# Kernel tuning notes

Measured on AMD Instinct MI355X. Metric: run time of the kernel, lower is better.

## Reference

```python
import jax, jax.numpy as jnp
import numpy as np

B, H1, W1 = 2, 64, 64
H2, W2 = 64, 64
DIM = 64    # query_latent_dim
CLD = 128   # cost_latent_dim
K = 8       # latent tokens in cost memory
HEADS = 8
CH = 1      # cost_heads_num
R = 4


def layer_norm(x, g, b, eps=1e-5):
    m = x.mean(-1, keepdims=True)
    v = ((x - m) ** 2).mean(-1, keepdims=True)
    return (x - m) / jnp.sqrt(v + eps) * g + b


def lin_pos_emb(x, dim):
    # LinearPositionEmbeddingSine: x [N,1,2] -> [N,1,dim]
    freq = jnp.linspace(0.0, dim // 4 - 1, dim // 4)
    a = 3.14 * x[..., 0:1] * freq / 200.0
    b = 3.14 * x[..., 1:2] * freq / 200.0
    return jnp.concatenate([jnp.sin(a), jnp.cos(a), jnp.sin(b), jnp.cos(b)], axis=-1)


def bilinear_sample(img, coords):
    # img: [N,C,H,W]; coords: [N,h,w,2] (x,y) pixel coords; zero padding, align_corners=True
    N, C, H, W = img.shape
    x, y = coords[..., 0], coords[..., 1]
    x0 = jnp.floor(x); y0 = jnp.floor(y)
    wx = x - x0; wy = y - y0
    nidx = jnp.arange(N)[:, None, None]

    def gather(xi, yi):
        valid = ((xi >= 0) & (xi <= W - 1) & (yi >= 0) & (yi <= H - 1)).astype(img.dtype)
        xc = jnp.clip(xi, 0, W - 1).astype(jnp.int32)
        yc = jnp.clip(yi, 0, H - 1).astype(jnp.int32)
        return img[nidx, :, yc, xc] * valid[..., None]  # [N,h,w,C]

    v00 = gather(x0, y0); v10 = gather(x0 + 1.0, y0)
    v01 = gather(x0, y0 + 1.0); v11 = gather(x0 + 1.0, y0 + 1.0)
    out = (v00 * ((1 - wx) * (1 - wy))[..., None] + v10 * (wx * (1 - wy))[..., None]
           + v01 * ((1 - wx) * wy)[..., None] + v11 * (wx * wy)[..., None])
    return out.transpose(0, 3, 1, 2)  # [N,C,h,w]


def encode_flow(cost_maps, coords1):
    b, _, h1, w1 = coords1.shape
    c = coords1.transpose(0, 2, 3, 1)  # [B,H1,W1,2]
    d = jnp.linspace(-float(R), float(R), 2 * R + 1)
    dy, dx = jnp.meshgrid(d, d, indexing='ij')
    delta = jnp.stack([dy, dx], axis=-1)  # [9,9,2]
    centroid = c.reshape(b * h1 * w1, 1, 1, 2)
    samp = centroid + delta[None]  # [B*H1*W1,9,9,2]
    corr = bilinear_sample(cost_maps, samp)  # [B*H1*W1,CH,9,9]
    return corr.reshape(b, h1, w1, -1).transpose(0, 3, 1, 2)  # [B,81*CH,H1,W1]


def upsample_flow(flow, mask):
    # convex upsample [H,W] -> [8H,8W]
    n, _, h, w = flow.shape
    m = jax.nn.softmax(mask.reshape(n, 1, 9, 8, 8, h, w), axis=2)
    f = jnp.pad(8.0 * flow, ((0, 0), (0, 0), (1, 1), (1, 1)))
    patches = jnp.stack([f[:, :, i:i + h, j:j + w] for i in range(3) for j in range(3)], axis=2)
    up = jnp.sum(m * patches[:, :, :, None, None], axis=2)  # [N,2,8,8,H,W]
    return up.transpose(0, 1, 4, 2, 5, 3).reshape(n, 2, 8 * h, 8 * w)


def setup_inputs() -> dict:
    key = jax.random.key(0)
    ks = jax.random.split(key, 16)
    Bn = B * H1 * W1
    ys, xs = np.meshgrid(np.arange(H1), np.arange(W1), indexing='ij')
    grid = jnp.asarray(np.stack([xs, ys], 0), jnp.float32)  # [2,H1,W1], (x,y)
    coords1 = jnp.broadcast_to(grid, (B, 2, H1, W1)) + 3.0 * jax.random.normal(ks[0], (B, 2, H1, W1), jnp.float32)
    s = 0.05
    return {
        'cost_maps': jax.random.normal(ks[1], (Bn, CH, H2, W2), jnp.float32),
        'cost_memory': jax.random.normal(ks[2], (Bn, K, CLD), jnp.float32),
        'coords1': coords1,
        'up_mask': jax.random.normal(ks[3], (B, 9 * 64, H1, W1), jnp.float32),
        'fte_w1': s * jax.random.normal(ks[4], (DIM, 81 * CH), jnp.float32),
        'fte_b1': jnp.zeros((DIM,), jnp.float32),
        'fte_w2': s * jax.random.normal(ks[5], (DIM, DIM), jnp.float32),
        'fte_b2': jnp.zeros((DIM,), jnp.float32),
        'ln1_g': jnp.ones((DIM,), jnp.float32),
        'ln1_b': jnp.zeros((DIM,), jnp.float32),
        'ln2_g': jnp.ones((DIM,), jnp.float32),
        'ln2_b': jnp.zeros((DIM,), jnp.float32),
        'wq': s * jax.random.normal(ks[6], (DIM, DIM), jnp.float32),
        'bq': jnp.zeros((DIM,), jnp.float32),
        'wk': s * jax.random.normal(ks[7], (CLD, DIM), jnp.float32),
        'bk': jnp.zeros((DIM,), jnp.float32),
        'wv': s * jax.random.normal(ks[8], (CLD, DIM), jnp.float32),
        'bv': jnp.zeros((DIM,), jnp.float32),
        'wp': s * jax.random.normal(ks[9], (2 * DIM, DIM), jnp.float32),
        'bp': jnp.zeros((DIM,), jnp.float32),
        'ffn_w1': s * jax.random.normal(ks[10], (DIM, DIM), jnp.float32),
        'ffn_b1': jnp.zeros((DIM,), jnp.float32),
        'ffn_w2': s * jax.random.normal(ks[11], (DIM, DIM), jnp.float32),
        'ffn_b2': jnp.zeros((DIM,), jnp.float32),
    }


def reference(cost_maps, cost_memory, coords1, up_mask,
              fte_w1, fte_b1, fte_w2, fte_b2,
              ln1_g, ln1_b, ln2_g, ln2_b,
              wq, bq, wk, bk, wv, bv, wp, bp,
              ffn_w1, ffn_b1, ffn_w2, ffn_b2):
    Bn = B * H1 * W1
    ys, xs = jnp.meshgrid(jnp.arange(H1, dtype=coords1.dtype), jnp.arange(W1, dtype=coords1.dtype), indexing='ij')
    coords0 = jnp.broadcast_to(jnp.stack([xs, ys], 0), (B, 2, H1, W1))

    # correlation-volume bilinear sampling (encode_flow_token)
    corr = encode_flow(cost_maps, coords1)  # [B,81*CH,H1,W1]

    # flow token encoder: 1x1 conv -> GELU -> 1x1 conv
    q = jnp.einsum('bchw,oc->bohw', corr, fte_w1) + fte_b1[None, :, None, None]
    q = jax.nn.gelu(q, approximate=False)
    q = jnp.einsum('bchw,oc->bohw', q, fte_w2) + fte_b2[None, :, None, None]
    query = q.transpose(0, 2, 3, 1).reshape(Bn, 1, DIM)

    # cross attention with linear sine position encoding of query coords
    qc = coords1.reshape(B, 2, H1 * W1).transpose(0, 2, 1).reshape(Bn, 1, 2)
    enc = lin_pos_emb(qc, DIM)
    short = query
    qn = layer_norm(query, ln1_g, ln1_b)
    qlin = (qn + enc) @ wq + bq            # [Bn,1,DIM]
    k = cost_memory @ wk + bk              # [Bn,K,DIM]
    v = cost_memory @ wv + bv
    hd = DIM // HEADS
    qh = qlin.reshape(Bn, 1, HEADS, hd).transpose(0, 2, 1, 3)
    kh = k.reshape(Bn, K, HEADS, hd).transpose(0, 2, 1, 3)
    vh = v.reshape(Bn, K, HEADS, hd).transpose(0, 2, 1, 3)
    attn = jax.nn.softmax(jnp.einsum('bhid,bhjd->bhij', qh, kh) * (hd ** -0.5), axis=-1)
    out = jnp.einsum('bhij,bhjd->bhid', attn, vh).transpose(0, 2, 1, 3).reshape(Bn, 1, DIM)
    x = jnp.concatenate([out, short], -1) @ wp + bp
    x = short + x
    xn = layer_norm(x, ln2_g, ln2_b)
    x = x + (jax.nn.gelu(xn @ ffn_w1 + ffn_b1, approximate=False) @ ffn_w2 + ffn_b2)
    cost_global = x.reshape(B, H1, W1, DIM).transpose(0, 3, 1, 2)

    # convex upsampling of the flow field
    flow_up = upsample_flow(coords1 - coords0, up_mask)  # [B,2,8*H1,8*W1]
    return (flow_up, cost_global)
```

## Files before the change

kernel.cpp:

```cpp
#include <hip/hip_runtime.h>
#include <math.h>

typedef _Float16 h2 __attribute__((ext_vector_type(2)));

#if __has_builtin(__builtin_amdgcn_fdot2)
#define FDOT2(a,b,c) __builtin_amdgcn_fdot2((a),(b),(c),false)
#else
__device__ __forceinline__ float FDOT2(h2 a, h2 b, float c){
    return c + (float)a.x*(float)b.x + (float)a.y*(float)b.y;
}
#endif

__device__ __forceinline__ h2 pk2(float x, float y){
#if __has_builtin(__builtin_amdgcn_cvt_pkrtz)
    return __builtin_bit_cast(h2, __builtin_amdgcn_cvt_pkrtz(x, y));
#else
    h2 r; r.x = (_Float16)x; r.y = (_Float16)y; return r;
#endif
}
__device__ __forceinline__ unsigned h2u(h2 v){ return __builtin_bit_cast(unsigned, v); }
__device__ __forceinline__ h2 uh2(unsigned v){ return __builtin_bit_cast(h2, v); }

__device__ __forceinline__ float fast_rcp(float x){
#if __has_builtin(__builtin_amdgcn_rcpf)
    return __builtin_amdgcn_rcpf(x);
#else
    return 1.f/x;
#endif
}

__device__ __forceinline__ float dot8(uint4 w, uint4 v, float acc){
    acc = FDOT2(uh2(w.x), uh2(v.x), acc);
    acc = FDOT2(uh2(w.y), uh2(v.y), acc);
    acc = FDOT2(uh2(w.z), uh2(v.z), acc);
    acc = FDOT2(uh2(w.w), uh2(v.w), acc);
    return acc;
}

__device__ __forceinline__ float gelu_exact(float x){
    return 0.5f * x * (1.0f + erff(x * 0.70710678118654752f));
}

__device__ __forceinline__ void ln_stats(float x, float& mean, float& inv){
    float s1 = x, s2 = x*x;
    #pragma unroll
    for(int off = 32; off >= 1; off >>= 1){
        s1 += __shfl_xor(s1, off, 64);
        s2 += __shfl_xor(s2, off, 64);
    }
    mean = s1 * (1.f/64.f);
    float var = fmaxf(s2 * (1.f/64.f) - mean*mean, 0.f);
    inv = rsqrtf(var + 1e-5f);
}

__device__ __forceinline__ void lds_fence(){ __asm__ volatile("s_waitcnt lgkmcnt(0)" ::: "memory"); }

#define W1T_OFF 0
#define W2T_OFF 2816
#define WQ_OFF  5120
#define FW1_OFF 7424
#define FW2_OFF 9728
#define WV_OFF  12032
#define WP_OFF  16384
#define WK_OFF  20736
#define WTOT    25344

#define CMO   0
#define TUO   544
#define CORRO 1088
#define QPO   1132
#define CCO   1168
#define PIXDW 1232
#define LDSDW (WTOT + 8*PIXDW)

__global__ void prep_weights(const float* __restrict__ w1, const float* __restrict__ w2,
                             const float* __restrict__ wq, const float* __restrict__ fw1,
                             const float* __restrict__ fw2, const float* __restrict__ wv,
                             const float* __restrict__ wp, const float* __restrict__ wk,
                             unsigned* __restrict__ ws){
    int idx = blockIdx.x * blockDim.x + threadIdx.x;
    if(idx >= WTOT) return;
    float a = 0.f, b = 0.f;
    if(idx < W2T_OFF){
        int t = idx / 44, cp = idx % 44;
        if(2*cp   < 81) a = w1[t*81 + 2*cp];
        if(2*cp+1 < 81) b = w1[t*81 + 2*cp+1];
    } else if(idx < WQ_OFF){
        int r = idx - W2T_OFF; int t = r / 36, cp = r % 36;
        if(cp < 32){ a = w2[t*64 + 2*cp]; b = w2[t*64 + 2*cp+1]; }
    } else if(idx < FW1_OFF){
        int r = idx - WQ_OFF; int t = r / 36, cp = r % 36;
        if(cp < 32){ a = wq[(2*cp)*64 + t]; b = wq[(2*cp+1)*64 + t]; }
    } else if(idx < FW2_OFF){
        int r = idx - FW1_OFF; int t = r / 36, cp = r % 36;
        if(cp < 32){ a = fw1[(2*cp)*64 + t]; b = fw1[(2*cp+1)*64 + t]; }
    } else if(idx < WV_OFF){
        int r = idx - FW2_OFF; int t = r / 36, cp = r % 36;
        if(cp < 32){ a = fw2[(2*cp)*64 + t]; b = fw2[(2*cp+1)*64 + t]; }
    } else if(idx < WP_OFF){
        int r = idx - WV_OFF; int t = r / 68, cp = r % 68;
        if(cp < 64){ a = wv[(2*cp)*64 + t]; b = wv[(2*cp+1)*64 + t]; }
    } else if(idx < WK_OFF){
        int r = idx - WP_OFF; int t = r / 68, cp = r % 68;
        if(cp < 64){ a = wp[(2*cp)*64 + t]; b = wp[(2*cp+1)*64 + t]; }
    } else {
        int r = idx - WK_OFF; int c = r / 36, hp = r % 36;
        if(hp < 32){ a = wk[c*64 + 2*hp]; b = wk[c*64 + 2*hp+1]; }
    }
    ws[idx] = h2u(pk2(a, b));
}

__device__ __forceinline__ float bilin(const float* __restrict__ cmap, float cx, float cy, int e){
    int i = e / 9, j = e - 9*i;
    float sx = cx + (float)(i - 4);
    float sy = cy + (float)(j - 4);
    float x0 = floorf(sx), y0 = floorf(sy);
    float wx = sx - x0,   wy = sy - y0;
    float acc = 0.f;
    #pragma unroll
    for(int dy = 0; dy < 2; dy++){
        #pragma unroll
        for(int dx = 0; dx < 2; dx++){
            float xf = x0 + (float)dx, yf = y0 + (float)dy;
            bool valid = (xf >= 0.f) && (xf <= 63.f) && (yf >= 0.f) && (yf <= 63.f);
            int xi = min(max((int)xf, 0), 63);
            int yi = min(max((int)yf, 0), 63);
            float v = valid ? cmap[yi*64 + xi] : 0.f;
            acc += v * ((dx ? wx : 1.f - wx) * (dy ? wy : 1.f - wy));
        }
    }
    return acc;
}

__global__ __launch_bounds__(512, 1) void decoder_main(
    const float* __restrict__ cost_maps, const float* __restrict__ cost_memory,
    const float* __restrict__ coords1, const unsigned* __restrict__ ws,
    const float* __restrict__ fte_b1, const float* __restrict__ fte_b2,
    const float* __restrict__ ln1_g, const float* __restrict__ ln1_b,
    const float* __restrict__ ln2_g, const float* __restrict__ ln2_b,
    const float* __restrict__ bq, const float* __restrict__ bv,
    const float* __restrict__ bp, const float* __restrict__ fb1,
    const float* __restrict__ fb2, float* __restrict__ out_cg)
{
    __shared__ unsigned sm[LDSDW];

    const int tid = threadIdx.x;
    const int wv  = tid >> 6;
    const int ln  = tid & 63;

    {
        const uint4* src = (const uint4*)ws;
        uint4* dst = (uint4*)sm;
        for(int i = tid; i < WTOT/4; i += 512) dst[i] = src[i];
    }
    const float b1v = fte_b1[ln], b2v = fte_b2[ln];
    const float g1v = ln1_g[ln], be1 = ln1_b[ln];
    const float g2v = ln2_g[ln], be2 = ln2_b[ln];
    const float bqv = bq[ln], bvv = bv[ln], bpv = bp[ln];
    const float f1v = fb1[ln], f2v = fb2[ln];
    __syncthreads();

    unsigned* P = sm + WTOT + wv * PIXDW;

    const int h_ = ln & 7;
    const int c0 = ln >> 3;
    const int j_ = ln >> 3;
    const int h3 = ln >> 3;

    int pix = blockIdx.x * 32 + wv;
    const float4* cm4p = (const float4*)cost_memory;
    float4 cmv0 = cm4p[(size_t)pix*256 +   0 + ln];
    float4 cmv1 = cm4p[(size_t)pix*256 +  64 + ln];
    float4 cmv2 = cm4p[(size_t)pix*256 + 128 + ln];
    float4 cmv3 = cm4p[(size_t)pix*256 + 192 + ln];
    float cx = coords1[(pix >> 12)*8192 + (pix & 4095)];
    float cy = coords1[(pix >> 12)*8192 + 4096 + (pix & 4095)];

    #pragma unroll 1
    for(int g = 0; g < 4; g++){
        {
            float4 v; int l0, jt, cp0;
            #define STAGE(V, I4) \
                v = V; l0 = 4*((I4)*64 + ln); jt = l0 >> 7; cp0 = (l0 & 127) >> 1; \
                { uint2 pw; pw.x = h2u(pk2(v.x, v.y)); pw.y = h2u(pk2(v.z, v.w)); \
                  *(uint2*)&P[CMO + jt*68 + cp0] = pw; }
            STAGE(cmv0, 0) STAGE(cmv1, 1) STAGE(cmv2, 2) STAGE(cmv3, 3)
            #undef STAGE
        }
        {
            const float* cmap = cost_maps + (size_t)pix * 4096;
            float cv = bilin(cmap, cx, cy, ln);
            float c2 = bilin(cmap, cx, cy, 64 + ln);
            float pr = __shfl_xor(cv, 1, 64);
            if((ln & 1) == 0) P[CORRO + (ln >> 1)] = h2u(pk2(cv, pr));
            float pr2 = __shfl_xor(c2, 1, 64);
            if(ln < 17 && (ln & 1) == 0){
                float bb = (ln == 16) ? 0.f : pr2;
                P[CORRO + 32 + (ln >> 1)] = h2u(pk2(c2, bb));
            }
            if(ln < 3) P[CORRO + 41 + ln] = 0u;
        }
        int npix = pix + 8;
        float4 n0, n1, n2, n3; float ncx = 0.f, ncy = 0.f;
        if(g < 3){
            n0 = cm4p[(size_t)npix*256 +   0 + ln];
            n1 = cm4p[(size_t)npix*256 +  64 + ln];
            n2 = cm4p[(size_t)npix*256 + 128 + ln];
            n3 = cm4p[(size_t)npix*256 + 192 + ln];
            ncx = coords1[(npix >> 12)*8192 + (npix & 4095)];
            ncy = coords1[(npix >> 12)*8192 + 4096 + (npix & 4095)];
        }
        lds_fence();

        float q1;
        {
            const uint4* wr = (const uint4*)&sm[W1T_OFF + ln*44];
            const uint4* ar = (const uint4*)&P[CORRO];
            float a0 = b1v, a1 = 0.f;
            #pragma unroll
            for(int gg = 0; gg < 10; gg += 2){
                a0 = dot8(wr[gg],   ar[gg],   a0);
                a1 = dot8(wr[gg+1], ar[gg+1], a1);
            }
            a0 = dot8(wr[10], ar[10], a0);
            q1 = a0 + a1;
        }
        q1 = gelu_exact(q1);
        {
            float pr = __shfl_xor(q1, 1, 64);
            if((ln & 1) == 0) P[QPO + (ln >> 1)] = h2u(pk2(q1, pr));
        }
        lds_fence();
        float shortv;
        {
            const uint4* wr = (const uint4*)&sm[W2T_OFF + ln*36];
            const uint4* ar = (const uint4*)&P[QPO];
            float a0 = b2v, a1 = 0.f;
            #pragma unroll
            for(int gg = 0; gg < 8; gg += 2){
                a0 = dot8(wr[gg],   ar[gg],   a0);
                a1 = dot8(wr[gg+1], ar[gg+1], a1);
            }
            shortv = a0 + a1;
        }
        {
            float psv = __shfl_xor(shortv, 1, 64);
            if((ln & 1) == 0) P[CCO + 32 + (ln >> 1)] = h2u(pk2(shortv, psv));
        }
        float mean, inv1;
        ln_stats(shortv, mean, inv1);
        float qn = (shortv - mean) * inv1 * g1v + be1;
        {
            int   fi    = ln & 15;
            float coord = (ln < 32) ? cx : cy;
            float ang   = 3.14f * coord * (float)fi / 200.0f;
            float enc   = (ln & 16) ? __cosf(ang) : __sinf(ang);
            float qv    = qn + enc;
            float pr = __shfl_xor(qv, 1, 64);
            if((ln & 1) == 0) P[QPO + (ln >> 1)] = h2u(pk2(qv, pr));
        }
        lds_fence();
        float qlin;
        {
            const uint4* wr = (const uint4*)&sm[WQ_OFF + ln*36];
            const uint4* ar = (const uint4*)&P[QPO];
            float a0 = bqv, a1 = 0.f;
            #pragma unroll
            for(int gg = 0; gg < 8; gg += 2){
                a0 = dot8(wr[gg],   ar[gg],   a0);
                a1 = dot8(wr[gg+1], ar[gg+1], a1);
            }
            qlin = a0 + a1;
        }
        (void)qlin;
        {
            uint4 qh4 = *(const uint4*)&P[QPO + h_*4];
            #pragma unroll
            for(int i = 0; i < 16; i++){
                int c = c0 + 8*i;
                uint4 wk4 = *(const uint4*)&sm[WK_OFF + c*36 + h_*4];
                float tv = dot8(wk4, qh4, 0.f);
                float prt = __shfl_xor(tv, 8, 64);
                if((c0 & 1) == 0) P[TUO + h_*68 + (c0 >> 1) + 4*i] = h2u(pk2(tv, prt));
            }
        }
        lds_fence();
        float sacc;
        {
            const int hk = ln & 7;
            const uint4* cmr = (const uint4*)&P[CMO + j_*68];
            const uint4* tur = (const uint4*)&P[TUO + hk*68];
            float s0 = 0.f, s1 = 0.f, s2 = 0.f, s3 = 0.f;
            #pragma unroll
            for(int gg = 0; gg < 16; gg += 4){
                s0 = dot8(cmr[gg],   tur[gg],   s0);
                s1 = dot8(cmr[gg+1], tur[gg+1], s1);
                s2 = dot8(cmr[gg+2], tur[gg+2], s2);
                s3 = dot8(cmr[gg+3], tur[gg+3], s3);
            }
            sacc = (s0 + s1) + (s2 + s3);
        }
        float p;
        {
            float sc = sacc * 0.35355339059327373f;
            float mx = sc;
            mx = fmaxf(mx, __shfl_xor(mx,  8, 64));
            mx = fmaxf(mx, __shfl_xor(mx, 16, 64));
            mx = fmaxf(mx, __shfl_xor(mx, 32, 64));
            float ex = __expf(sc - mx);
            float se = ex;
            se += __shfl_xor(se,  8, 64);
            se += __shfl_xor(se, 16, 64);
            se += __shfl_xor(se, 32, 64);
            p = ex * fast_rcp(se);
        }
        {
            float av[8];
            #pragma unroll
            for(int j = 0; j < 8; j++) av[j] = __shfl(p, j*8 + h_, 64);
            h2 u0 = pk2(0.f,0.f), u1 = u0, u2 = u0, u3 = u0;
            h2 u4 = u0, u5 = u0, u6 = u0, u7 = u0;
            #pragma unroll
            for(int j = 0; j < 8; j++){
                h2 aj = pk2(av[j], av[j]);
                const uint4* cmr = (const uint4*)&P[CMO + j*68 + 8*c0];
                uint4 qa = cmr[0], qb = cmr[1];
                u0 += aj * uh2(qa.x); u1 += aj * uh2(qa.y);
                u2 += aj * uh2(qa.z); u3 += aj * uh2(qa.w);
                u4 += aj * uh2(qb.x); u5 += aj * uh2(qb.y);
                u6 += aj * uh2(qb.z); u7 += aj * uh2(qb.w);
            }
            uint4 wa; wa.x = h2u(u0); wa.y = h2u(u1); wa.z = h2u(u2); wa.w = h2u(u3);
            uint4 wb; wb.x = h2u(u4); wb.y = h2u(u5); wb.z = h2u(u6); wb.w = h2u(u7);
            *(uint4*)&P[TUO + h_*68 + 8*c0]     = wa;
            *(uint4*)&P[TUO + h_*68 + 8*c0 + 4] = wb;
        }
        lds_fence();
        float attno;
        {
            const uint4* ur = (const uint4*)&P[TUO + h3*68];
            const uint4* wr = (const uint4*)&sm[WV_OFF + ln*68];
            float a0 = bvv, a1 = 0.f, a2 = 0.f, a3 = 0.f;
            #pragma unroll
            for(int gg = 0; gg < 16; gg += 4){
                a0 = dot8(ur[gg],   wr[gg],   a0);
                a1 = dot8(ur[gg+1], wr[gg+1], a1);
                a2 = dot8(ur[gg+2], wr[gg+2], a2);
                a3 = dot8(ur[gg+3], wr[gg+3], a3);
            }
            attno = (a0 + a1) + (a2 + a3);
        }
        {
            float pa = __shfl_xor(attno, 1, 64);
            if((ln & 1) == 0) P[CCO + (ln >> 1)] = h2u(pk2(attno, pa));
        }
        lds_fence();
        float x;
        {
            const uint4* wr = (const uint4*)&sm[WP_OFF + ln*68];
            const uint4* ar = (const uint4*)&P[CCO];
            float a0 = bpv, a1 = 0.f, a2 = 0.f, a3 = 0.f;
            #pragma unroll
            for(int gg = 0; gg < 16; gg += 4){
                a0 = dot8(wr[gg],   ar[gg],   a0);
                a1 = dot8(wr[gg+1], ar[gg+1], a1);
                a2 = dot8(wr[gg+2], ar[gg+2], a2);
                a3 = dot8(wr[gg+3], ar[gg+3], a3);
            }
            x = (a0 + a1) + (a2 + a3);
        }
        x += shortv;
        float m2, inv2;
        ln_stats(x, m2, inv2);
        float xn = (x - m2) * inv2 * g2v + be2;
        {
            float pr = __shfl_xor(xn, 1, 64);
            if((ln & 1) == 0) P[QPO + (ln >> 1)] = h2u(pk2(xn, pr));
        }
        lds_fence();
        float h1v;
        {
            const uint4* wr = (const uint4*)&sm[FW1_OFF + ln*36];
            const uint4* ar = (const uint4*)&P[QPO];
            float a0 = f1v, a1 = 0.f;
            #pragma unroll
            for(int gg = 0; gg < 8; gg += 2){
                a0 = dot8(wr[gg],   ar[gg],   a0);
                a1 = dot8(wr[gg+1], ar[gg+1], a1);
            }
            h1v = a0 + a1;
        }
        h1v = gelu_exact(h1v);
        {
            float pr = __shfl_xor(h1v, 1, 64);
            if((ln & 1) == 0) P[QPO + (ln >> 1)] = h2u(pk2(h1v, pr));
        }
        lds_fence();
        float f2;
        {
            const uint4* wr = (const uint4*)&sm[FW2_OFF + ln*36];
            const uint4* ar = (const uint4*)&P[QPO];
            float a0 = f2v, a1 = 0.f;
            #pragma unroll
            for(int gg = 0; gg < 8; gg += 2){
                a0 = dot8(wr[gg],   ar[gg],   a0);
                a1 = dot8(wr[gg+1], ar[gg+1], a1);
            }
            f2 = a0 + a1;
        }
        x += f2;
        {
            int bb = pix >> 12, hh = (pix >> 6) & 63, ww = pix & 63;
            out_cg[(((size_t)(bb*64 + ln))*64 + hh)*64 + ww] = x;
        }
        pix = npix; cx = ncx; cy = ncy;
        cmv0 = n0; cmv1 = n1; cmv2 = n2; cmv3 = n3;
    }
}

__global__ __launch_bounds__(512) void upsample_kernel(
    const float* __restrict__ coords1, const float* __restrict__ up_mask,
    float* __restrict__ out)
{
    __shared__ float mtile[9 * 544];
    __shared__ float fxs[3 * 64];
    __shared__ float fys[3 * 64];

    const int r = blockIdx.x & 7;
    const int h = (blockIdx.x >> 3) & 63;
    const int b = blockIdx.x >> 9;
    const int id = threadIdx.x;

    {
        const int s_ = id >> 6, w_ = id & 63;
        #pragma unroll
        for(int k = 0; k < 9; k++){
            int c = k*64 + r*8 + s_;
            mtile[k*544 + s_*68 + w_] =
                up_mask[(((size_t)b*576 + c)*64 + h)*64 + w_];
        }
    }
    if(id < 192){
        const int i = id >> 6, w_ = id & 63;
        const int hh = h + i - 1;
        float fx = 0.f, fy = 0.f;
        if(hh >= 0 && hh < 64){
            fx = 8.f * (coords1[((b*2 + 0)*64 + hh)*64 + w_] - (float)w_);
            fy = 8.f * (coords1[((b*2 + 1)*64 + hh)*64 + w_] - (float)hh);
        }
        fxs[i*64 + w_] = fx;
        fys[i*64 + w_] = fy;
    }
    __syncthreads();

    const int w = id >> 3, s = id & 7;
    float m[9];
    #pragma unroll
    for(int k = 0; k < 9; k++) m[k] = mtile[k*544 + s*68 + w];
    float mx = m[0];
    #pragma unroll
    for(int k = 1; k < 9; k++) mx = fmaxf(mx, m[k]);
    float se = 0.f;
    #pragma unroll
    for(int k = 0; k < 9; k++){ m[k] = __expf(m[k] - mx); se += m[k]; }
    float inv = fast_rcp(se);

    float ox = 0.f, oy = 0.f;
    #pragma unroll
    for(int k = 0; k < 9; k++){
        int i = k / 3, j = k % 3;
        int ww = w + j - 1;
        float fx = 0.f, fy = 0.f;
        if(ww >= 0 && ww < 64){
            fx = fxs[i*64 + ww];
            fy = fys[i*64 + ww];
        }
        ox += m[k] * fx;
        oy += m[k] * fy;
    }
    ox *= inv; oy *= inv;

    const size_t row = (size_t)(h*8 + r) * 512 + w*8 + s;
    out[(size_t)(b*2 + 0)*262144 + row] = ox;
    out[(size_t)(b*2 + 1)*262144 + row] = oy;
}

extern "C" void kernel_launch(void* const* d_in, const int* in_sizes, int n_in,
                              void* d_out, int out_size, void* d_ws, size_t ws_size,
                              hipStream_t stream)
{
    const float* cost_maps   = (const float*)d_in[0];
    const float* cost_memory = (const float*)d_in[1];
    const float* coords1     = (const float*)d_in[2];
    const float* up_mask     = (const float*)d_in[3];
    const float* fte_w1      = (const float*)d_in[4];
    const float* fte_b1      = (const float*)d_in[5];
    const float* fte_w2      = (const float*)d_in[6];
    const float* fte_b2      = (const float*)d_in[7];
    const float* ln1_g       = (const float*)d_in[8];
    const float* ln1_b       = (const float*)d_in[9];
    const float* ln2_g       = (const float*)d_in[10];
    const float* ln2_b       = (const float*)d_in[11];
    const float* wq          = (const float*)d_in[12];
    const float* bq          = (const float*)d_in[13];
    const float* wk          = (const float*)d_in[14];
    const float* bv          = (const float*)d_in[17];
    const float* wv          = (const float*)d_in[16];
    const float* wp          = (const float*)d_in[18];
    const float* bp          = (const float*)d_in[19];
    const float* fw1         = (const float*)d_in[20];
    const float* fb1         = (const float*)d_in[21];
    const float* fw2         = (const float*)d_in[22];
    const float* fb2         = (const float*)d_in[23];
    float* out = (float*)d_out;
    unsigned* wsu = (unsigned*)d_ws;

    prep_weights<<<(WTOT + 511)/512, 512, 0, stream>>>(
        fte_w1, fte_w2, wq, fw1, fw2, wv, wp, wk, wsu);

    decoder_main<<<256, 512, 0, stream>>>(cost_maps, cost_memory, coords1, wsu,
        fte_b1, fte_b2, ln1_g, ln1_b, ln2_g, ln2_b,
        bq, bv, bp, fb1, fb2,
        out + 2*2*512*512);

    upsample_kernel<<<2*64*8, 512, 0, stream>>>(coords1, up_mask, out);
}
```

Measured before the change: 266.0 us.

## Fuse weight prep and convex upsampling into the main decoder kernel

Drops the separate weight-prep and upsample launches. Each block now packs and transposes the weights into LDS straight from the raw global tensors. The convex-upsample work runs at the tail of the decoder kernel, using wave shuffles in place of an LDS tile, and writes float4 outputs. This removes two launches and the workspace round trip. The cost is that every block repeats the strided weight gathers, and the upsample now runs on only 256 resident blocks. It also starts feeding the projected query qlin into the attention step, which the old code computed and then discarded, so it changes numerics and adds an LDS store and fence.

Measured after the change: 279.6 us. 1.05x slower.

```diff
diff --git a/kernel.cpp b/kernel.cpp
--- a/kernel.cpp
+++ b/kernel.cpp
@@ -72,43 +72,6 @@
 #define CCO   1168
 #define PIXDW 1232
 #define LDSDW (WTOT + 8*PIXDW)
-
-__global__ void prep_weights(const float* __restrict__ w1, const float* __restrict__ w2,
-                             const float* __restrict__ wq, const float* __restrict__ fw1,
-                             const float* __restrict__ fw2, const float* __restrict__ wv,
-                             const float* __restrict__ wp, const float* __restrict__ wk,
-                             unsigned* __restrict__ ws){
-    int idx = blockIdx.x * blockDim.x + threadIdx.x;
-    if(idx >= WTOT) return;
-    float a = 0.f, b = 0.f;
-    if(idx < W2T_OFF){
-        int t = idx / 44, cp = idx % 44;
-        if(2*cp   < 81) a = w1[t*81 + 2*cp];
-        if(2*cp+1 < 81) b = w1[t*81 + 2*cp+1];
-    } else if(idx < WQ_OFF){
-        int r = idx - W2T_OFF; int t = r / 36, cp = r % 36;
-        if(cp < 32){ a = w2[t*64 + 2*cp]; b = w2[t*64 + 2*cp+1]; }
-    } else if(idx < FW1_OFF){
-        int r = idx - WQ_OFF; int t = r / 36, cp = r % 36;
-        if(cp < 32){ a = wq[(2*cp)*64 + t]; b = wq[(2*cp+1)*64 + t]; }
-    } else if(idx < FW2_OFF){
-        int r = idx - FW1_OFF; int t = r / 36, cp = r % 36;
-        if(cp < 32){ a = fw1[(2*cp)*64 + t]; b = fw1[(2*cp+1)*64 + t]; }
-    } else if(idx < WV_OFF){
-        int r = idx - FW2_OFF; int t = r / 36, cp = r % 36;
-        if(cp < 32){ a = fw2[(2*cp)*64 + t]; b = fw2[(2*cp+1)*64 + t]; }
-    } else if(idx < WP_OFF){
-        int r = idx - WV_OFF; int t = r / 68, cp = r % 68;
-        if(cp < 64){ a = wv[(2*cp)*64 + t]; b = wv[(2*cp+1)*64 + t]; }
-    } else if(idx < WK_OFF){
-        int r = idx - WP_OFF; int t = r / 68, cp = r % 68;
-        if(cp < 64){ a = wp[(2*cp)*64 + t]; b = wp[(2*cp+1)*64 + t]; }
-    } else {
-        int r = idx - WK_OFF; int c = r / 36, hp = r % 36;
-        if(hp < 32){ a = wk[c*64 + 2*hp]; b = wk[c*64 + 2*hp+1]; }
-    }
-    ws[idx] = h2u(pk2(a, b));
-}
 
 __device__ __forceinline__ float bilin(const float* __restrict__ cmap, float cx, float cy, int e){
     int i = e / 9, j = e - 9*i;
@@ -132,15 +95,19 @@
     return acc;
 }
 
-__global__ __launch_bounds__(512, 1) void decoder_main(
+__global__ __launch_bounds__(512, 1) void decoder_fused(
     const float* __restrict__ cost_maps, const float* __restrict__ cost_memory,
-    const float* __restrict__ coords1, const unsigned* __restrict__ ws,
+    const float* __restrict__ coords1, const float* __restrict__ up_mask,
+    const float* __restrict__ w1, const float* __restrict__ w2,
+    const float* __restrict__ wq, const float* __restrict__ fw1,
+    const float* __restrict__ fw2, const float* __restrict__ wvm,
+    const float* __restrict__ wpm, const float* __restrict__ wkm,
     const float* __restrict__ fte_b1, const float* __restrict__ fte_b2,
     const float* __restrict__ ln1_g, const float* __restrict__ ln1_b,
     const float* __restrict__ ln2_g, const float* __restrict__ ln2_b,
     const float* __restrict__ bq, const float* __restrict__ bv,
     const float* __restrict__ bp, const float* __restrict__ fb1,
-    const float* __restrict__ fb2, float* __restrict__ out_cg)
+    const float* __restrict__ fb2, float* __restrict__ out)
 {
     __shared__ unsigned sm[LDSDW];
 
@@ -148,10 +115,35 @@
     const int wv  = tid >> 6;
     const int ln  = tid & 63;
 
-    {
-        const uint4* src = (const uint4*)ws;
-        uint4* dst = (uint4*)sm;
-        for(int i = tid; i < WTOT/4; i += 512) dst[i] = src[i];
+    for(int idx = tid; idx < WTOT; idx += 512){
+        float a = 0.f, b = 0.f;
+        if(idx < W2T_OFF){
+            int t = idx / 44, cp = idx % 44;
+            if(2*cp   < 81) a = w1[t*81 + 2*cp];
+            if(2*cp+1 < 81) b = w1[t*81 + 2*cp+1];
+        } else if(idx < WQ_OFF){
+            int r = idx - W2T_OFF; int t = r / 36, cp = r % 36;
+            if(cp < 32){ a = w2[t*64 + 2*cp]; b = w2[t*64 + 2*cp+1]; }
+        } else if(idx < FW1_OFF){
+            int r = idx - WQ_OFF; int t = r / 36, cp = r % 36;
+            if(cp < 32){ a = wq[(2*cp)*64 + t]; b = wq[(2*cp+1)*64 + t]; }
+        } else if(idx < FW2_OFF){
+            int r = idx - FW1_OFF; int t = r / 36, cp = r % 36;
+            if(cp < 32){ a = fw1[(2*cp)*64 + t]; b = fw1[(2*cp+1)*64 + t]; }
+        } else if(idx < WV_OFF){
+            int r = idx - FW2_OFF; int t = r / 36, cp = r % 36;
+            if(cp < 32){ a = fw2[(2*cp)*64 + t]; b = fw2[(2*cp+1)*64 + t]; }
+        } else if(idx < WP_OFF){
+            int r = idx - WV_OFF; int t = r / 68, cp = r % 68;
+            if(cp < 64){ a = wvm[(2*cp)*64 + t]; b = wvm[(2*cp+1)*64 + t]; }
+        } else if(idx < WK_OFF){
+            int r = idx - WP_OFF; int t = r / 68, cp = r % 68;
+            if(cp < 64){ a = wpm[(2*cp)*64 + t]; b = wpm[(2*cp+1)*64 + t]; }
+        } else {
+            int r = idx - WK_OFF; int c = r / 36, hp = r % 36;
+            if(hp < 32){ a = wkm[c*64 + 2*hp]; b = wkm[c*64 + 2*hp+1]; }
+        }
+        sm[idx] = h2u(pk2(a, b));
     }
     const float b1v = fte_b1[ln], b2v = fte_b2[ln];
     const float g1v = ln1_g[ln], be1 = ln1_b[ln];
@@ -160,6 +152,7 @@
     const float f1v = fb1[ln], f2v = fb2[ln];
     __syncthreads();
 
+    float* out_cg = out + 2*2*512*512;
     unsigned* P = sm + WTOT + wv * PIXDW;
 
     const int h_ = ln & 7;
@@ -272,7 +265,11 @@
             }
             qlin = a0 + a1;
         }
-        (void)qlin;
+        {
+            float pr = __shfl_xor(qlin, 1, 64);
+            if((ln & 1) == 0) P[QPO + (ln >> 1)] = h2u(pk2(qlin, pr));
+        }
+        lds_fence();
         {
             uint4 qh4 = *(const uint4*)&P[QPO + h_*4];
             #pragma unroll
@@ -416,73 +413,68 @@
         pix = npix; cx = ncx; cy = ncy;
         cmv0 = n0; cmv1 = n1; cmv2 = n2; cmv3 = n3;
     }
-}
-
-__global__ __launch_bounds__(512) void upsample_kernel(
-    const float* __restrict__ coords1, const float* __restrict__ up_mask,
-    float* __restrict__ out)
-{
-    __shared__ float mtile[9 * 544];
-    __shared__ float fxs[3 * 64];
-    __shared__ float fys[3 * 64];
-
-    const int r = blockIdx.x & 7;
-    const int h = (blockIdx.x >> 3) & 63;
-    const int b = blockIdx.x >> 9;
-    const int id = threadIdx.x;
 
     {
-        const int s_ = id >> 6, w_ = id & 63;
+        const int U  = blockIdx.x * 4 + (wv >> 1);
+        const int sh = (wv & 1) * 4;
+        const int ub = U >> 9, uh = (U >> 3) & 63, ur = U & 7;
+        const int w  = ln;
+
+        float fx[3], fy[3];
+        #pragma unroll
+        for(int i = 0; i < 3; i++){
+            int hh = uh + i - 1;
+            bool ok = (hh >= 0) && (hh < 64);
+            int hc = min(max(hh, 0), 63);
+            float cxv = coords1[((ub*2 + 0)*64 + hc)*64 + w];
+            float cyv = coords1[((ub*2 + 1)*64 + hc)*64 + w];
+            fx[i] = ok ? 8.f * (cxv - (float)w)  : 0.f;
+            fy[i] = ok ? 8.f * (cyv - (float)hh) : 0.f;
+        }
+        float fxm[3], fxp[3], fym[3], fyp[3];
+        #pragma unroll
+        for(int i = 0; i < 3; i++){
+            fxm[i] = __shfl(fx[i], w - 1, 64);
+            fxp[i] = __shfl(fx[i], w + 1, 64);
+            fym[i] = __shfl(fy[i], w - 1, 64);
+            fyp[i] = __shfl(fy[i], w + 1, 64);
+            if(w == 0) { fxm[i] = 0.f; fym[i] = 0.f; }
+            if(w == 63){ fxp[i] = 0.f; fyp[i] = 0.f; }
+        }
+        float m[36];
         #pragma unroll
         for(int k = 0; k < 9; k++){
-            int c = k*64 + r*8 + s_;
-            mtile[k*544 + s_*68 + w_] =
-                up_mask[(((size_t)b*576 + c)*64 + h)*64 + w_];
-        }
+            #pragma unroll
+            for(int si = 0; si < 4; si++){
+                int c = k*64 + ur*8 + sh + si;
+                m[k*4 + si] = up_mask[(((size_t)ub*576 + c)*64 + uh)*64 + w];
+            }
+        }
+        float outx[4], outy[4];
+        #pragma unroll
+        for(int si = 0; si < 4; si++){
+            float mx = m[si];
+            #pragma unroll
+            for(int k = 1; k < 9; k++) mx = fmaxf(mx, m[k*4 + si]);
+            float e, se = 0.f, ox = 0.f, oy = 0.f;
+            #pragma unroll
+            for(int k = 0; k < 9; k++){
+                e = __expf(m[k*4 + si] - mx);
+                se += e;
+                int i = k / 3, j = k % 3;
+                float fxv = (j == 0) ? fxm[i] : ((j == 1) ? fx[i] : fxp[i]);
+                float fyv = (j == 0) ? fym[i] : ((j == 1) ? fy[i] : fyp[i]);
+                ox += e * fxv;
+                oy += e * fyv;
+            }
+            float inv = fast_rcp(se);
+            outx[si] = ox * inv;
+            outy[si] = oy * inv;
+        }
+        size_t row = (size_t)(uh*8 + ur) * 512 + w*8 + sh;
+        *(float4*)&out[(size_t)(ub*2 + 0)*262144 + row] = *(const float4*)outx;
+        *(float4*)&out[(size_t)(ub*2 + 1)*262144 + row] = *(const float4*)outy;
     }
-    if(id < 192){
-        const int i = id >> 6, w_ = id & 63;
-        const int hh = h + i - 1;
-        float fx = 0.f, fy = 0.f;
-        if(hh >= 0 && hh < 64){
-            fx = 8.f * (coords1[((b*2 + 0)*64 + hh)*64 + w_] - (float)w_);
-            fy = 8.f * (coords1[((b*2 + 1)*64 + hh)*64 + w_] - (float)hh);
-        }
-        fxs[i*64 + w_] = fx;
-        fys[i*64 + w_] = fy;
-    }
-    __syncthreads();
-
-    const int w = id >> 3, s = id & 7;
-    float m[9];
-    #pragma unroll
-    for(int k = 0; k < 9; k++) m[k] = mtile[k*544 + s*68 + w];
-    float mx = m[0];
-    #pragma unroll
-    for(int k = 1; k < 9; k++) mx = fmaxf(mx, m[k]);
-    float se = 0.f;
-    #pragma unroll
-    for(int k = 0; k < 9; k++){ m[k] = __expf(m[k] - mx); se += m[k]; }
-    float inv = fast_rcp(se);
-
-    float ox = 0.f, oy = 0.f;
-    #pragma unroll
-    for(int k = 0; k < 9; k++){
-        int i = k / 3, j = k % 3;
-        int ww = w + j - 1;
-        float fx = 0.f, fy = 0.f;
-        if(ww >= 0 && ww < 64){
-            fx = fxs[i*64 + ww];
-            fy = fys[i*64 + ww];
-        }
-        ox += m[k] * fx;
-        oy += m[k] * fy;
-    }
-    ox *= inv; oy *= inv;
-
-    const size_t row = (size_t)(h*8 + r) * 512 + w*8 + s;
-    out[(size_t)(b*2 + 0)*262144 + row] = ox;
-    out[(size_t)(b*2 + 1)*262144 + row] = oy;
 }
 
 extern "C" void kernel_launch(void* const* d_in, const int* in_sizes, int n_in,
@@ -513,15 +505,12 @@
     const float* fw2         = (const float*)d_in[22];
     const float* fb2         = (const float*)d_in[23];
     float* out = (float*)d_out;
-    unsigned* wsu = (unsigned*)d_ws;
-
-    prep_weights<<<(WTOT + 511)/512, 512, 0, stream>>>(
-        fte_w1, fte_w2, wq, fw1, fw2, wv, wp, wk, wsu);
-
-    decoder_main<<<256, 512, 0, stream>>>(cost_maps, cost_memory, coords1, wsu,
+    (void)d_ws; (void)ws_size;
+
+    decoder_fused<<<256, 512, 0, stream>>>(
+        cost_maps, cost_memory, coords1, up_mask,
+        fte_w1, fte_w2, wq, fw1, fw2, wv, wp, wk,
         fte_b1, fte_b2, ln1_g, ln1_b, ln2_g, ln2_b,
         bq, bv, bp, fb1, fb2,
-        out + 2*2*512*512);
-
-    upsample_kernel<<<2*64*8, 512, 0, stream>>>(coords1, up_mask, out);
-}
+        out);
+}
```
